# Kernel optimization log

Hardware: AMD Instinct MI355X
Metric: run time of the kernel (lower is better)

Reference implementation:

```python
import jax, jax.numpy as jnp
import numpy as np

N_FREQS = 6  # PositionEmbedding default used by LISA


def setup_inputs() -> dict:
    key = jax.random.key(0)
    ks = jax.random.split(key, 8)
    B, L, N, D, H = 8, 32768, 2048, 64, 256
    in_dim = 1 * (2 * N_FREQS + 1) + 3 * D  # 13 + 192 = 205

    def w(k, i, o):
        return jax.random.normal(k, (i, o), jnp.float32) * (1.0 / np.sqrt(i))

    return {
        "coord": jax.random.uniform(ks[0], (B, L, 1), jnp.float32),
        "latent": jax.random.normal(ks[1], (B, N, D), jnp.float32),
        "W0": w(ks[2], in_dim, H), "b0": jnp.zeros((H,), jnp.float32),
        "W1": w(ks[3], H, H), "b1": jnp.zeros((H,), jnp.float32),
        "W2": w(ks[4], H, H), "b2": jnp.zeros((H,), jnp.float32),
        "W3": w(ks[5], H, H), "b3": jnp.zeros((H,), jnp.float32),
        "W4": w(ks[6], H, 1), "b4": jnp.zeros((1,), jnp.float32),
    }


def reference(coord, latent, W0, b0, W1, b1, W2, b2, W3, b3, W4, b4):
    B, N, D = latent.shape
    # feat_unfold: concat shifted-prev / self / shifted-next along channels
    feat = jnp.swapaxes(latent, 1, 2)                                   # [B, D, N]
    feat_prev = jnp.concatenate([feat[:, :, :1], feat[:, :, :-1]], axis=2)
    feat_next = jnp.concatenate([feat[:, :, 1:], feat[:, :, -1:]], axis=2)
    feat = jnp.concatenate([feat_prev, feat, feat_next], axis=1)        # [B, 3D, N]

    # grid_sample(bilinear, padding_mode='border', align_corners=False) on a
    # 1-row image: y coordinate 0 hits row 0 exactly, so only x interpolates.
    # torch mapping: ix = ((gx + 1) * W - 1) / 2 with gx = coord*2 - 1
    ix = coord[..., 0] * N - 0.5                                        # [B, L]
    x0 = jnp.floor(ix)
    t = ix - x0                                                         # lerp weight
    i0 = jnp.clip(x0.astype(jnp.int32), 0, N - 1)                       # border clamp
    i1 = jnp.clip(x0.astype(jnp.int32) + 1, 0, N - 1)
    f0 = jnp.take_along_axis(feat, i0[:, None, :], axis=2)              # [B, 3D, L]
    f1 = jnp.take_along_axis(feat, i1[:, None, :], axis=2)
    sampled = (1.0 - t)[:, None, :] * f0 + t[:, None, :] * f1
    sampled = jnp.swapaxes(sampled, 1, 2)                               # [B, L, 3D]

    # positional encoding: [x, sin(f x), cos(f x) for f in 1,2,4,8,16,32]
    freqs = 2.0 ** jnp.arange(N_FREQS, dtype=jnp.float32)
    ang = coord * freqs                                                 # [B, L, 6]
    pe = jnp.stack([jnp.sin(ang), jnp.cos(ang)], axis=-1)
    pe = pe.reshape(ang.shape[0], ang.shape[1], 2 * N_FREQS)            # [B, L, 12]

    inp = jnp.concatenate([coord, pe, sampled], axis=-1)                # [B, L, 205]

    h = jax.nn.relu(inp @ W0 + b0)
    h = jax.nn.relu(h @ W1 + b1)
    h = jax.nn.relu(h @ W2 + b2)
    h = jax.nn.relu(h @ W3 + b3)
    return h @ W4 + b4                                                  # [B, L, 1]
```

## Files before the change

### kernel.cpp

```cpp
#include <hip/hip_runtime.h>
#include <hip/hip_bf16.h>

typedef unsigned short ushort_t;
typedef unsigned int uint_t;
typedef __attribute__((ext_vector_type(8))) short short8;
typedef __attribute__((ext_vector_type(4))) float float4v;
typedef __attribute__((ext_vector_type(4))) uint_t uint4v;

#define NLAT 2048
#define DLAT 64

#define PW_BASE 128
#define PW0_OFF 0
#define PW1_OFF 57344
#define PW2_OFF 122880
#define PW3_OFF 188416

__device__ __forceinline__ float b2f(ushort_t u) {
  union { uint_t i; float f; } v; v.i = ((uint_t)u) << 16; return v.f;
}
__device__ __forceinline__ ushort_t f2b(float f) {
  uint_t x = __float_as_uint(f);
  uint_t r = (x + 0x7fffu + ((x >> 16) & 1u)) >> 16;
  return (ushort_t)r;
}
__device__ __forceinline__ uint_t pack2(float lo, float hi) {
  float2 t; t.x = lo; t.y = hi;
  union { __hip_bfloat162 h; uint_t u; } cv;
  cv.h = __float22bfloat162_rn(t);
  return cv.u;
}
__device__ __forceinline__ int imin(int a, int b) { return a < b ? a : b; }
__device__ __forceinline__ int imax(int a, int b) { return a > b ? a : b; }

__device__ __forceinline__ float ldv(const float* p, long i)    { return p[i]; }
__device__ __forceinline__ float ldv(const ushort_t* p, long i) { return b2f(p[i]); }
__device__ __forceinline__ void stv(float* p, long i, float v)    { p[i] = v; }
__device__ __forceinline__ void stv(ushort_t* p, long i, float v) { p[i] = f2b(v); }

__device__ __forceinline__ float4 load4f(const float* p) { return *(const float4*)p; }
__device__ __forceinline__ float4 load4f(const ushort_t* p) {
  uint2 u = *(const uint2*)p;
  float4 r;
  r.x = b2f((ushort_t)(u.x & 0xffffu)); r.y = b2f((ushort_t)(u.x >> 16));
  r.z = b2f((ushort_t)(u.y & 0xffffu)); r.w = b2f((ushort_t)(u.y >> 16));
  return r;
}

__global__ void detect_mode(const ushort_t* __restrict__ lat, int* __restrict__ flag) {
  if (threadIdx.x == 0) *flag = 0;
  __syncthreads();
  int big = 0;
  for (int i = threadIdx.x; i < 1024; i += 64) {
    float v = b2f(lat[i]);
    if (!(fabsf(v) < 1e5f)) big = 1;
  }
  if (__any(big) && threadIdx.x == 0) *flag = 1;
}

template <typename TI>
__global__ void pack_w_t(const TI* __restrict__ W0, const TI* __restrict__ W1,
                         const TI* __restrict__ W2, const TI* __restrict__ W3,
                         ushort_t* __restrict__ pw, const int* __restrict__ flag, int want)
{
  if (*flag != want) return;
  int g = blockIdx.x * blockDim.x + threadIdx.x;
  if (g >= 31 * 1024) return;
  int lane = g & 63, q = lane >> 4;
  int mt   = (g >> 6) & 15;
  int ktg  = g >> 10;
  const TI* W; ushort_t* dst; int kt, KT; bool isw0 = false;
  if (ktg < 7)       { W = W0; dst = pw + PW0_OFF; kt = ktg;      KT = 7; isw0 = true; }
  else if (ktg < 15) { W = W1; dst = pw + PW1_OFF; kt = ktg - 7;  KT = 8; }
  else if (ktg < 23) { W = W2; dst = pw + PW2_OFF; kt = ktg - 15; KT = 8; }
  else               { W = W3; dst = pw + PW3_OFF; kt = ktg - 23; KT = 8; }
  int col = mt * 16 + (lane & 15);
  uint_t words[4];
#pragma unroll
  for (int h = 0; h < 4; ++h) {
    ushort_t vv[2];
#pragma unroll
    for (int e = 0; e < 2; ++e) {
      int j = 2 * h + e;
      int f = 32 * kt + 16 * (j >> 2) + 4 * q + (j & 3);
      int row = f;
      if (isw0) row = (f < 192) ? (13 + f) : (f == 192 ? 0 : (f <= 204 ? f - 192 : -1));
      vv[e] = (row >= 0) ? f2b(ldv(W, (long)row * 256 + col)) : (ushort_t)0;
    }
    words[h] = (uint_t)vv[0] | ((uint_t)vv[1] << 16);
  }
  uint4 o; o.x = words[0]; o.y = words[1]; o.z = words[2]; o.w = words[3];
  *(uint4*)(dst + ((size_t)(mt * KT + kt) * 64 + lane) * 8) = o;
}

template <int KT>
__device__ __forceinline__ void run_layer_new(const ushort_t* __restrict__ pwl,
                                              float4v (&acc)[4][8],
                                              const ushort_t* __restrict__ act,
                                              int lane, int wv)
{
#pragma unroll
  for (int m = 0; m < 4; ++m)
#pragma unroll
    for (int p = 0; p < 8; ++p)
      acc[m][p] = (float4v){0.f, 0.f, 0.f, 0.f};

  const ushort_t* abase = pwl + (((size_t)(4 * wv) * KT) * 64 + lane) * 8;

  short8 A0[4], A1[4];
#pragma unroll
  for (int m = 0; m < 4; ++m)
    A0[m] = *(const short8*)(abase + (size_t)(m * KT) * 512);

#pragma unroll
  for (int kt = 0; kt < KT; ++kt) {
    short8 (&Ac)[4] = (kt & 1) ? A1 : A0;
    short8 (&An)[4] = (kt & 1) ? A0 : A1;
    if (kt + 1 < KT) {
#pragma unroll
      for (int m = 0; m < 4; ++m)
        An[m] = *(const short8*)(abase + (size_t)(m * KT + kt + 1) * 512);
    }
#pragma unroll
    for (int p = 0; p < 8; ++p) {
      short8 B = *(const short8*)&act[((size_t)(p * 8 + kt) * 64 + lane) * 8];
      acc[0][p] = __builtin_amdgcn_mfma_f32_16x16x32_bf16(Ac[0], B, acc[0][p], 0, 0, 0);
      acc[1][p] = __builtin_amdgcn_mfma_f32_16x16x32_bf16(Ac[1], B, acc[1][p], 0, 0, 0);
      acc[2][p] = __builtin_amdgcn_mfma_f32_16x16x32_bf16(Ac[2], B, acc[2][p], 0, 0, 0);
      acc[3][p] = __builtin_amdgcn_mfma_f32_16x16x32_bf16(Ac[3], B, acc[3][p], 0, 0, 0);
    }
  }
}

__device__ __forceinline__ void convert_store(float4v (&acc)[4][8],
                                              ushort_t* __restrict__ act,
                                              const float* __restrict__ bwl,
                                              int lane, int wv, int q)
{
  __syncthreads();
#pragma unroll
  for (int p2 = 0; p2 < 2; ++p2) {
    const float4 bE = *(const float4*)&bwl[wv * 64 + p2 * 32 + 4 * q];
    const float4 bO = *(const float4*)&bwl[wv * 64 + p2 * 32 + 16 + 4 * q];
    const int kt = 2 * wv + p2;
#pragma unroll
    for (int p = 0; p < 8; ++p) {
      const float4v& aE = acc[2 * p2][p];
      const float4v& aO = acc[2 * p2 + 1][p];
      uint4 o;
      o.x = pack2(fmaxf(aE[0] + bE.x, 0.f), fmaxf(aE[1] + bE.y, 0.f));
      o.y = pack2(fmaxf(aE[2] + bE.z, 0.f), fmaxf(aE[3] + bE.w, 0.f));
      o.z = pack2(fmaxf(aO[0] + bO.x, 0.f), fmaxf(aO[1] + bO.y, 0.f));
      o.w = pack2(fmaxf(aO[2] + bO.z, 0.f), fmaxf(aO[3] + bO.w, 0.f));
      *(uint4*)&act[((size_t)(p * 8 + kt) * 64 + lane) * 8] = o;
    }
  }
  __syncthreads();
}

template <typename TI>
__global__ __launch_bounds__(256, 2) void lisa_fused_t(
    const TI* __restrict__ coord, const TI* __restrict__ latent,
    const TI* __restrict__ bias0, const TI* __restrict__ bias1,
    const TI* __restrict__ bias2, const TI* __restrict__ bias3,
    const TI* __restrict__ W4,    const TI* __restrict__ b4,
    const ushort_t* __restrict__ pw, TI* __restrict__ out,
    const int* __restrict__ flag, int want)
{
  if (*flag != want) return;
  __shared__ __align__(16) ushort_t act[8 * 8 * 64 * 8];
  __shared__ __align__(16) float bw[4 * 256 + 256 + 1];

  const int tid  = threadIdx.x;
  const int lane = tid & 63, q = lane >> 4, m15 = lane & 15;
  const int wv   = tid >> 6;
  const long pbase = (long)blockIdx.x * 128 + wv * 32 + m15;

  for (int i = tid; i < 1281; i += 256) {
    float v;
    if (i < 256)       v = ldv(bias0, i);
    else if (i < 512)  v = ldv(bias1, i - 256);
    else if (i < 768)  v = ldv(bias2, i - 512);
    else if (i < 1024) v = ldv(bias3, i - 768);
    else if (i < 1280) v = ldv(W4, i - 1024);
    else               v = ldv(b4, 0);
    bw[i] = v;
  }

  uint4v hu[7][2];
#pragma unroll
  for (int g = 0; g < 2; ++g) {
    long p = pbase + g * 16;
    float c   = ldv(coord, p);
    float ixv = c * 2048.0f - 0.5f;
    float x0f = floorf(ixv);
    float t   = ixv - x0f;
    int   x0  = (int)x0f;
    int   i0  = imin(imax(x0, 0), NLAT - 1);
    int   i1  = imin(imax(x0 + 1, 0), NLAT - 1);
    float w0 = 1.0f - t, w1 = t;
    int rows0[3] = { imax(i0 - 1, 0), i0, imin(i0 + 1, NLAT - 1) };
    int rows1[3] = { imax(i1 - 1, 0), i1, imin(i1 + 1, NLAT - 1) };
    const TI* lat = latent + (size_t)(p >> 15) * (NLAT * DLAT);
#pragma unroll
    for (int tb = 0; tb < 12; ++tb) {
      int region = tb >> 2;
      int d0 = 16 * (tb & 3) + 4 * q;
      float4 a = load4f(lat + (long)rows0[region] * DLAT + d0);
      float4 b = load4f(lat + (long)rows1[region] * DLAT + d0);
      hu[tb >> 1][g][(tb & 1) * 2 + 0] = pack2(w0 * a.x + w1 * b.x, w0 * a.y + w1 * b.y);
      hu[tb >> 1][g][(tb & 1) * 2 + 1] = pack2(w0 * a.z + w1 * b.z, w0 * a.w + w1 * b.w);
    }
    float pv[4];
#pragma unroll
    for (int s = 0; s < 4; ++s) {
      int f = 192 + 4 * q + s;
      float v = 0.0f;
      if (f == 192) v = c;
      else if (f <= 204) {
        int i = f - 193;
        float fr = (float)(1 << (i >> 1));
        float ang = c * fr;
        v = (i & 1) ? __cosf(ang) : __sinf(ang);
      }
      pv[s] = v;
    }
    hu[6][g][0] = pack2(pv[0], pv[1]);
    hu[6][g][1] = pack2(pv[2], pv[3]);
    hu[6][g][2] = 0; hu[6][g][3] = 0;

    const int pt = 2 * wv + g;
#pragma unroll
    for (int kt = 0; kt < 7; ++kt)
      *(uint4v*)&act[((size_t)(pt * 8 + kt) * 64 + lane) * 8] = hu[kt][g];
  }
  __syncthreads();

  float4v acc[4][8];

  run_layer_new<7>(pw + PW0_OFF, acc, act, lane, wv);
  convert_store(acc, act, bw + 0 * 256, lane, wv, q);
  run_layer_new<8>(pw + PW1_OFF, acc, act, lane, wv);
  convert_store(acc, act, bw + 1 * 256, lane, wv, q);
  run_layer_new<8>(pw + PW2_OFF, acc, act, lane, wv);
  convert_store(acc, act, bw + 2 * 256, lane, wv, q);
  run_layer_new<8>(pw + PW3_OFF, acc, act, lane, wv);

  __syncthreads();

  float psum[8];
#pragma unroll
  for (int p = 0; p < 8; ++p) psum[p] = 0.f;
#pragma unroll
  for (int m = 0; m < 4; ++m) {
    const float4 b3v = *(const float4*)&bw[3 * 256 + wv * 64 + m * 16 + 4 * q];
    const float4 w4v = *(const float4*)&bw[1024 + wv * 64 + m * 16 + 4 * q];
#pragma unroll
    for (int p = 0; p < 8; ++p) {
      float v;
      v = fmaxf(acc[m][p][0] + b3v.x, 0.f); psum[p] += v * w4v.x;
      v = fmaxf(acc[m][p][1] + b3v.y, 0.f); psum[p] += v * w4v.y;
      v = fmaxf(acc[m][p][2] + b3v.z, 0.f); psum[p] += v * w4v.z;
      v = fmaxf(acc[m][p][3] + b3v.w, 0.f); psum[p] += v * w4v.w;
    }
  }
#pragma unroll
  for (int p = 0; p < 8; ++p) {
    psum[p] += __shfl_xor(psum[p], 16, 64);
    psum[p] += __shfl_xor(psum[p], 32, 64);
  }
  float* part = (float*)act;
  if (lane < 16) {
#pragma unroll
    for (int p = 0; p < 8; ++p) part[wv * 128 + p * 16 + lane] = psum[p];
  }
  __syncthreads();
  if (tid < 128) {
    float s = part[tid] + part[128 + tid] + part[256 + tid] + part[384 + tid]
            + bw[1280];
    stv(out, (long)blockIdx.x * 128 + tid, s);
  }
}

extern "C" void kernel_launch(void* const* d_in, const int* in_sizes, int n_in,
                              void* d_out, int out_size, void* d_ws, size_t ws_size,
                              hipStream_t stream) {
  int* flag = (int*)d_ws;
  ushort_t* pw = (ushort_t*)d_ws + PW_BASE;

  detect_mode<<<1, 64, 0, stream>>>((const ushort_t*)d_in[1], flag);

  pack_w_t<float><<<62, 512, 0, stream>>>(
      (const float*)d_in[2], (const float*)d_in[4], (const float*)d_in[6],
      (const float*)d_in[8], pw, flag, 1);
  lisa_fused_t<float><<<2048, 256, 0, stream>>>(
      (const float*)d_in[0], (const float*)d_in[1],
      (const float*)d_in[3], (const float*)d_in[5], (const float*)d_in[7],
      (const float*)d_in[9], (const float*)d_in[10], (const float*)d_in[11],
      pw, (float*)d_out, flag, 1);

  pack_w_t<ushort_t><<<62, 512, 0, stream>>>(
      (const ushort_t*)d_in[2], (const ushort_t*)d_in[4], (const ushort_t*)d_in[6],
      (const ushort_t*)d_in[8], pw, flag, 0);
  lisa_fused_t<ushort_t><<<2048, 256, 0, stream>>>(
      (const ushort_t*)d_in[0], (const ushort_t*)d_in[1],
      (const ushort_t*)d_in[3], (const ushort_t*)d_in[5], (const ushort_t*)d_in[7],
      (const ushort_t*)d_in[9], (const ushort_t*)d_in[10], (const ushort_t*)d_in[11],
      pw, (ushort_t*)d_out, flag, 0);
}
```

Before: 221.5 us.

## Halve points per block, raise occupancy, prefetch next-layer weights, lighten barriers

Each block now processes 64 points instead of 128, so the accumulator array, shared activation buffer and grid size change accordingly, and launch bounds rise to 3 blocks per CU to improve latency hiding. The first weight fragment of each layer is prefetched before the preceding convert/barrier. Some __syncthreads calls are replaced with raw s_barrier plus explicit waitcnt. In exchange, each weight fragment loaded from global or L2 now feeds half as many MFMAs, so weight traffic per point roughly doubles.

After: 227.6 us. +2.8%, slower.

```diff
diff --git a/kernel.cpp b/kernel.cpp
--- a/kernel.cpp
+++ b/kernel.cpp
@@ -94,23 +94,29 @@
 }
 
 template <int KT>
-__device__ __forceinline__ void run_layer_new(const ushort_t* __restrict__ pwl,
-                                              float4v (&acc)[4][8],
-                                              const ushort_t* __restrict__ act,
-                                              int lane, int wv)
-{
-#pragma unroll
-  for (int m = 0; m < 4; ++m)
-#pragma unroll
-    for (int p = 0; p < 8; ++p)
-      acc[m][p] = (float4v){0.f, 0.f, 0.f, 0.f};
-
+__device__ __forceinline__ void prefetch_A0(const ushort_t* __restrict__ pwl,
+                                            short8 (&A0)[4], int lane, int wv)
+{
   const ushort_t* abase = pwl + (((size_t)(4 * wv) * KT) * 64 + lane) * 8;
-
-  short8 A0[4], A1[4];
 #pragma unroll
   for (int m = 0; m < 4; ++m)
     A0[m] = *(const short8*)(abase + (size_t)(m * KT) * 512);
+}
+
+template <int KT>
+__device__ __forceinline__ void run_layer_new(const ushort_t* __restrict__ pwl,
+                                              float4v (&acc)[4][4],
+                                              const ushort_t* __restrict__ act,
+                                              int lane, int wv, short8 (&A0)[4])
+{
+#pragma unroll
+  for (int m = 0; m < 4; ++m)
+#pragma unroll
+    for (int p = 0; p < 4; ++p)
+      acc[m][p] = (float4v){0.f, 0.f, 0.f, 0.f};
+
+  const ushort_t* abase = pwl + (((size_t)(4 * wv) * KT) * 64 + lane) * 8;
+  short8 A1[4];
 
 #pragma unroll
   for (int kt = 0; kt < KT; ++kt) {
@@ -122,7 +128,7 @@
         An[m] = *(const short8*)(abase + (size_t)(m * KT + kt + 1) * 512);
     }
 #pragma unroll
-    for (int p = 0; p < 8; ++p) {
+    for (int p = 0; p < 4; ++p) {
       short8 B = *(const short8*)&act[((size_t)(p * 8 + kt) * 64 + lane) * 8];
       acc[0][p] = __builtin_amdgcn_mfma_f32_16x16x32_bf16(Ac[0], B, acc[0][p], 0, 0, 0);
       acc[1][p] = __builtin_amdgcn_mfma_f32_16x16x32_bf16(Ac[1], B, acc[1][p], 0, 0, 0);
@@ -132,19 +138,20 @@
   }
 }
 
-__device__ __forceinline__ void convert_store(float4v (&acc)[4][8],
+__device__ __forceinline__ void convert_store(float4v (&acc)[4][4],
                                               ushort_t* __restrict__ act,
                                               const float* __restrict__ bwl,
                                               int lane, int wv, int q)
 {
-  __syncthreads();
+  asm volatile("" ::: "memory");
+  __builtin_amdgcn_s_barrier();
 #pragma unroll
   for (int p2 = 0; p2 < 2; ++p2) {
     const float4 bE = *(const float4*)&bwl[wv * 64 + p2 * 32 + 4 * q];
     const float4 bO = *(const float4*)&bwl[wv * 64 + p2 * 32 + 16 + 4 * q];
     const int kt = 2 * wv + p2;
 #pragma unroll
-    for (int p = 0; p < 8; ++p) {
+    for (int p = 0; p < 4; ++p) {
       const float4v& aE = acc[2 * p2][p];
       const float4v& aO = acc[2 * p2 + 1][p];
       uint4 o;
@@ -155,11 +162,12 @@
       *(uint4*)&act[((size_t)(p * 8 + kt) * 64 + lane) * 8] = o;
     }
   }
-  __syncthreads();
+  asm volatile("s_waitcnt lgkmcnt(0)" ::: "memory");
+  __builtin_amdgcn_s_barrier();
 }
 
 template <typename TI>
-__global__ __launch_bounds__(256, 2) void lisa_fused_t(
+__global__ __launch_bounds__(256, 3) void lisa_fused_t(
     const TI* __restrict__ coord, const TI* __restrict__ latent,
     const TI* __restrict__ bias0, const TI* __restrict__ bias1,
     const TI* __restrict__ bias2, const TI* __restrict__ bias3,
@@ -168,13 +176,16 @@
     const int* __restrict__ flag, int want)
 {
   if (*flag != want) return;
-  __shared__ __align__(16) ushort_t act[8 * 8 * 64 * 8];
+  __shared__ __align__(16) ushort_t act[4 * 8 * 64 * 8];
   __shared__ __align__(16) float bw[4 * 256 + 256 + 1];
 
   const int tid  = threadIdx.x;
   const int lane = tid & 63, q = lane >> 4, m15 = lane & 15;
   const int wv   = tid >> 6;
-  const long pbase = (long)blockIdx.x * 128 + wv * 32 + m15;
+  const long pbase = (long)blockIdx.x * 64 + wv * 16 + m15;
+
+  short8 A0[4];
+  prefetch_A0<7>(pw + PW0_OFF, A0, lane, wv);
 
   for (int i = tid; i < 1281; i += 256) {
     float v;
@@ -187,10 +198,8 @@
     bw[i] = v;
   }
 
-  uint4v hu[7][2];
-#pragma unroll
-  for (int g = 0; g < 2; ++g) {
-    long p = pbase + g * 16;
+  {
+    const long p = pbase;
     float c   = ldv(coord, p);
     float ixv = c * 2048.0f - 0.5f;
     float x0f = floorf(ixv);
@@ -202,14 +211,15 @@
     int rows0[3] = { imax(i0 - 1, 0), i0, imin(i0 + 1, NLAT - 1) };
     int rows1[3] = { imax(i1 - 1, 0), i1, imin(i1 + 1, NLAT - 1) };
     const TI* lat = latent + (size_t)(p >> 15) * (NLAT * DLAT);
+    uint4v hu[7];
 #pragma unroll
     for (int tb = 0; tb < 12; ++tb) {
       int region = tb >> 2;
       int d0 = 16 * (tb & 3) + 4 * q;
       float4 a = load4f(lat + (long)rows0[region] * DLAT + d0);
       float4 b = load4f(lat + (long)rows1[region] * DLAT + d0);
-      hu[tb >> 1][g][(tb & 1) * 2 + 0] = pack2(w0 * a.x + w1 * b.x, w0 * a.y + w1 * b.y);
-      hu[tb >> 1][g][(tb & 1) * 2 + 1] = pack2(w0 * a.z + w1 * b.z, w0 * a.w + w1 * b.w);
+      hu[tb >> 1][(tb & 1) * 2 + 0] = pack2(w0 * a.x + w1 * b.x, w0 * a.y + w1 * b.y);
+      hu[tb >> 1][(tb & 1) * 2 + 1] = pack2(w0 * a.z + w1 * b.z, w0 * a.w + w1 * b.w);
     }
     float pv[4];
 #pragma unroll
@@ -225,38 +235,36 @@
       }
       pv[s] = v;
     }
-    hu[6][g][0] = pack2(pv[0], pv[1]);
-    hu[6][g][1] = pack2(pv[2], pv[3]);
-    hu[6][g][2] = 0; hu[6][g][3] = 0;
-
-    const int pt = 2 * wv + g;
+    hu[6][0] = pack2(pv[0], pv[1]);
+    hu[6][1] = pack2(pv[2], pv[3]);
+    hu[6][2] = 0; hu[6][3] = 0;
+
 #pragma unroll
     for (int kt = 0; kt < 7; ++kt)
-      *(uint4v*)&act[((size_t)(pt * 8 + kt) * 64 + lane) * 8] = hu[kt][g];
+      *(uint4v*)&act[((size_t)(wv * 8 + kt) * 64 + lane) * 8] = hu[kt];
   }
   __syncthreads();
 
-  float4v acc[4][8];
-
-  run_layer_new<7>(pw + PW0_OFF, acc, act, lane, wv);
+  float4v acc[4][4];
+
+  run_layer_new<7>(pw + PW0_OFF, acc, act, lane, wv, A0);
+  prefetch_A0<8>(pw + PW1_OFF, A0, lane, wv);
   convert_store(acc, act, bw + 0 * 256, lane, wv, q);
-  run_layer_new<8>(pw + PW1_OFF, acc, act, lane, wv);
+  run_layer_new<8>(pw + PW1_OFF, acc, act, lane, wv, A0);
+  prefetch_A0<8>(pw + PW2_OFF, A0, lane, wv);
   convert_store(acc, act, bw + 1 * 256, lane, wv, q);
-  run_layer_new<8>(pw + PW2_OFF, acc, act, lane, wv);
+  run_layer_new<8>(pw + PW2_OFF, acc, act, lane, wv, A0);
+  prefetch_A0<8>(pw + PW3_OFF, A0, lane, wv);
   convert_store(acc, act, bw + 2 * 256, lane, wv, q);
-  run_layer_new<8>(pw + PW3_OFF, acc, act, lane, wv);
-
-  __syncthreads();
-
-  float psum[8];
-#pragma unroll
-  for (int p = 0; p < 8; ++p) psum[p] = 0.f;
+  run_layer_new<8>(pw + PW3_OFF, acc, act, lane, wv, A0);
+
+  float psum[4] = {0.f, 0.f, 0.f, 0.f};
 #pragma unroll
   for (int m = 0; m < 4; ++m) {
     const float4 b3v = *(const float4*)&bw[3 * 256 + wv * 64 + m * 16 + 4 * q];
     const float4 w4v = *(const float4*)&bw[1024 + wv * 64 + m * 16 + 4 * q];
 #pragma unroll
-    for (int p = 0; p < 8; ++p) {
+    for (int p = 0; p < 4; ++p) {
       float v;
       v = fmaxf(acc[m][p][0] + b3v.x, 0.f); psum[p] += v * w4v.x;
       v = fmaxf(acc[m][p][1] + b3v.y, 0.f); psum[p] += v * w4v.y;
@@ -265,20 +273,23 @@
     }
   }
 #pragma unroll
-  for (int p = 0; p < 8; ++p) {
+  for (int p = 0; p < 4; ++p) {
     psum[p] += __shfl_xor(psum[p], 16, 64);
     psum[p] += __shfl_xor(psum[p], 32, 64);
   }
+
+  asm volatile("" ::: "memory");
+  __builtin_amdgcn_s_barrier();
   float* part = (float*)act;
   if (lane < 16) {
 #pragma unroll
-    for (int p = 0; p < 8; ++p) part[wv * 128 + p * 16 + lane] = psum[p];
+    for (int p = 0; p < 4; ++p) part[wv * 64 + p * 16 + lane] = psum[p];
   }
   __syncthreads();
-  if (tid < 128) {
-    float s = part[tid] + part[128 + tid] + part[256 + tid] + part[384 + tid]
+  if (tid < 64) {
+    float s = part[tid] + part[64 + tid] + part[128 + tid] + part[192 + tid]
             + bw[1280];
-    stv(out, (long)blockIdx.x * 128 + tid, s);
+    stv(out, (long)blockIdx.x * 64 + tid, s);
   }
 }
 
@@ -293,7 +304,7 @@
   pack_w_t<float><<<62, 512, 0, stream>>>(
       (const float*)d_in[2], (const float*)d_in[4], (const float*)d_in[6],
       (const float*)d_in[8], pw, flag, 1);
-  lisa_fused_t<float><<<2048, 256, 0, stream>>>(
+  lisa_fused_t<float><<<4096, 256, 0, stream>>>(
       (const float*)d_in[0], (const float*)d_in[1],
       (const float*)d_in[3], (const float*)d_in[5], (const float*)d_in[7],
       (const float*)d_in[9], (const float*)d_in[10], (const float*)d_in[11],
@@ -302,7 +313,7 @@
   pack_w_t<ushort_t><<<62, 512, 0, stream>>>(
       (const ushort_t*)d_in[2], (const ushort_t*)d_in[4], (const ushort_t*)d_in[6],
       (const ushort_t*)d_in[8], pw, flag, 0);
-  lisa_fused_t<ushort_t><<<2048, 256, 0, stream>>>(
+  lisa_fused_t<ushort_t><<<4096, 256, 0, stream>>>(
       (const ushort_t*)d_in[0], (const ushort_t*)d_in[1],
       (const ushort_t*)d_in[3], (const ushort_t*)d_in[5], (const ushort_t*)d_in[7],
       (const ushort_t*)d_in[9], (const ushort_t*)d_in[10], (const ushort_t*)d_in[11],
```
